# Optimization experiments

Measured on AMD Instinct MI355X. Metric: run time of the kernel, lower is better.

The kernel has to match this reference:

```python
import jax, jax.numpy as jnp
import numpy as np

B, S, D = 4, 1568, 1024
H = 16
HD = D // H  # 64


def setup_inputs() -> dict:
    key = jax.random.key(0)
    ks = jax.random.split(key, 9)
    scale = 0.02
    return {
        "hidden_states": jax.random.normal(ks[0], (B, S, D), dtype=jnp.float32),
        "Wq": jax.random.normal(ks[1], (D, D), dtype=jnp.float32) * scale,
        "bq": jnp.zeros((D,), dtype=jnp.float32),
        "Wk": jax.random.normal(ks[2], (D, D), dtype=jnp.float32) * scale,
        "bk": jnp.zeros((D,), dtype=jnp.float32),
        "Wv": jax.random.normal(ks[3], (D, D), dtype=jnp.float32) * scale,
        "bv": jnp.zeros((D,), dtype=jnp.float32),
        "Wp": jax.random.normal(ks[4], (D, D), dtype=jnp.float32) * scale,
        "bp": jnp.zeros((D,), dtype=jnp.float32),
    }


def reference(hidden_states, Wq, bq, Wk, bk, Wv, bv, Wp, bp):
    x = hidden_states  # [B, S, D]
    # Linear projections (torch Linear: x @ W.T + b)
    q = x @ Wq.T + bq
    k = x @ Wk.T + bk
    v = x @ Wv.T + bv
    # split heads: [B, H, S, HD]
    def heads(t):
        return t.reshape(B, S, H, HD).transpose(0, 2, 1, 3)
    q, k, v = heads(q), heads(k), heads(v)
    scale = 1.0 / jnp.sqrt(jnp.asarray(HD, dtype=q.dtype))
    scores = jnp.einsum('bhqd,bhkd->bhqk', q, k) * scale  # [B,H,S,S]
    probs = jax.nn.softmax(scores, axis=-1)
    ctx = jnp.einsum('bhqk,bhkd->bhqd', probs, v)  # [B,H,S,HD]
    ctx = ctx.transpose(0, 2, 1, 3).reshape(B, S, D)
    out = ctx @ Wp.T + bp
    return out
```

## Files before the change

### kernel.cpp

```cpp
#include <hip/hip_runtime.h>
#include <stdint.h>

#define SEQ 1568
#define SEQV 1600
#define DIM 1024
#define NB 4
#define NH 16
#define HD 64

typedef unsigned short u16;
typedef __bf16 bf16x8 __attribute__((ext_vector_type(8)));
typedef float f32x4 __attribute__((ext_vector_type(4)));

#define QSCALE 0.18033688011112042f

#define PSTR 72

__device__ __forceinline__ void load_lds16(const u16* g, u16* s) {
  __builtin_amdgcn_global_load_lds((__attribute__((address_space(1))) void*)g,
                                   (__attribute__((address_space(3))) void*)s,
                                   16, 0, 0);
}

__global__ __launch_bounds__(256) void cvt_all(
    const float* __restrict__ x,  const float* __restrict__ wq,
    const float* __restrict__ wk, const float* __restrict__ wv,
    const float* __restrict__ wp,
    u16* __restrict__ xb, u16* __restrict__ wqb, u16* __restrict__ wkb,
    u16* __restrict__ wvb, u16* __restrict__ wpb) {
  int i = blockIdx.x * 256 + threadIdx.x;
  const float* src; u16* dst; int off;
  if (i < 1605632)      { src = x;  dst = xb;  off = i; }
  else if (i < 1867776) { src = wq; dst = wqb; off = i - 1605632; }
  else if (i < 2129920) { src = wk; dst = wkb; off = i - 1867776; }
  else if (i < 2392064) { src = wv; dst = wvb; off = i - 2129920; }
  else                  { src = wp; dst = wpb; off = i - 2392064; }
  float4 v = ((const float4*)src)[off];
  union { unsigned long long u; __bf16 h[4]; } o;
  o.h[0] = (__bf16)v.x; o.h[1] = (__bf16)v.y;
  o.h[2] = (__bf16)v.z; o.h[3] = (__bf16)v.w;
  ((unsigned long long*)dst)[off] = o.u;
}

__global__ __launch_bounds__(256) void gemm_qkv(
    const u16* __restrict__ xb,
    const u16* __restrict__ wq, const u16* __restrict__ wk, const u16* __restrict__ wv,
    const float* __restrict__ bq, const float* __restrict__ bk, const float* __restrict__ bv,
    u16* __restrict__ qo, u16* __restrict__ ko, u16* __restrict__ vto) {
  const int z = blockIdx.z;
  const u16* W = (z == 0) ? wq : (z == 1) ? wk : wv;
  const float* bias = (z == 0) ? bq : (z == 1) ? bk : bv;

  __shared__ __align__(16) u16 sA[128 * 32];
  __shared__ __align__(16) u16 sB[128 * 32];

  const int tid = threadIdx.x;
  const int wave = tid >> 6;
  const int lane = tid & 63;
  const int l15 = lane & 15;
  const int quad = lane >> 4;
  const int bi = blockIdx.y / 13;
  const int st = blockIdx.y % 13;
  const int bn = blockIdx.x * 128;
  const int wm = (wave >> 1) * 64;
  const int wn = (wave & 1) * 64;

  const int sr = lane >> 2;
  const int sc = (lane & 3) * 8;
  const int r0 = wave * 32;

  f32x4 acc[4][4] = {};

  for (int k0 = 0; k0 < DIM; k0 += 32) {
    __syncthreads();
    {
      int sr1 = st * 128 + r0 + sr;       if (sr1 >= SEQ) sr1 = SEQ - 1;
      int sr2 = st * 128 + r0 + 16 + sr;  if (sr2 >= SEQ) sr2 = SEQ - 1;
      load_lds16(xb + (size_t)(bi * SEQ + sr1) * DIM + k0 + sc, &sA[r0 * 32]);
      load_lds16(xb + (size_t)(bi * SEQ + sr2) * DIM + k0 + sc, &sA[(r0 + 16) * 32]);
      const u16* gB = W + (size_t)(bn + r0 + sr) * DIM + k0 + sc;
      load_lds16(gB, &sB[r0 * 32]);
      load_lds16(gB + 16 * DIM, &sB[(r0 + 16) * 32]);
    }
    __syncthreads();

    bf16x8 a[4], b[4];
#pragma unroll
    for (int mt = 0; mt < 4; mt++)
      a[mt] = *(const bf16x8*)&sA[(wm + mt * 16 + l15) * 32 + quad * 8];
#pragma unroll
    for (int nt = 0; nt < 4; nt++)
      b[nt] = *(const bf16x8*)&sB[(wn + nt * 16 + l15) * 32 + quad * 8];
#pragma unroll
    for (int mt = 0; mt < 4; mt++)
#pragma unroll
      for (int nt = 0; nt < 4; nt++)
        acc[mt][nt] = __builtin_amdgcn_mfma_f32_16x16x32_bf16(a[mt], b[nt], acc[mt][nt], 0, 0, 0);
  }

#pragma unroll
  for (int nt = 0; nt < 4; nt++) {
    const int n = bn + wn + nt * 16 + l15;
    const float bia = bias[n];
    const int h = n >> 6, d = n & 63;
#pragma unroll
    for (int mt = 0; mt < 4; mt++) {
      const int sbase = st * 128 + wm + mt * 16 + quad * 4;
#pragma unroll
      for (int r = 0; r < 4; r++) {
        const int s = sbase + r;
        if (s < SEQ) {
          float val = acc[mt][nt][r] + bia;
          if (z == 0) val *= QSCALE;
          const __bf16 o = (__bf16)val;
          if (z == 0)
            *(__bf16*)&qo[(((size_t)(bi * NH + h)) * SEQ + s) * HD + d] = o;
          else if (z == 1)
            *(__bf16*)&ko[(((size_t)(bi * NH + h)) * SEQ + s) * HD + d] = o;
          else
            *(__bf16*)&vto[(((size_t)(bi * NH + h)) * HD + d) * SEQV + s] = o;
        }
      }
    }
  }
}

__global__ __launch_bounds__(256, 4) void attn(
    const u16* __restrict__ q, const u16* __restrict__ k,
    const u16* __restrict__ vt, u16* __restrict__ ctx) {
  const int bh = blockIdx.y;
  const int qt = blockIdx.x;
  const int tid = threadIdx.x;
  const int wave = tid >> 6, lane = tid & 63, l15 = lane & 15, quad = lane >> 4;

  __shared__ __align__(16) u16 sK[64 * 64];
  __shared__ __align__(16) u16 sV[64 * 64];
  __shared__ __align__(16) u16 sP[4][32 * PSTR];

  const u16* qh = q + (size_t)bh * (SEQ * HD);
  const u16* kh = k + (size_t)bh * (SEQ * HD);
  const u16* vh = vt + (size_t)bh * (HD * SEQV);

  bf16x8 aq[2][2];
#pragma unroll
  for (int mt = 0; mt < 2; mt++) {
    int qrow = qt * 128 + wave * 32 + mt * 16 + l15;
    int qr = qrow < SEQ ? qrow : SEQ - 1;
    aq[mt][0] = *(const bf16x8*)&qh[(size_t)qr * HD + quad * 8];
    aq[mt][1] = *(const bf16x8*)&qh[(size_t)qr * HD + 32 + quad * 8];
  }

  f32x4 o[2][4] = {};
  float lrow[2][4] = {};

  const int jrow = lane >> 3;
  const int cg = (lane & 7) ^ jrow;
  u16* sPw = sP[wave];
  const int j7 = l15 & 7;

  for (int j0 = 0; j0 < 1536; j0 += 64) {
    __syncthreads();
    load_lds16(&kh[(size_t)(j0 + wave * 16 + jrow) * HD + cg * 8], &sK[(wave * 16) * 64]);
    load_lds16(&kh[(size_t)(j0 + wave * 16 + 8 + jrow) * HD + cg * 8], &sK[(wave * 16 + 8) * 64]);
    load_lds16(&vh[(size_t)(wave * 16 + jrow) * SEQV + j0 + cg * 8], &sV[(wave * 16) * 64]);
    load_lds16(&vh[(size_t)(wave * 16 + 8 + jrow) * SEQV + j0 + cg * 8], &sV[(wave * 16 + 8) * 64]);
    __syncthreads();

#pragma unroll
    for (int mt = 0; mt < 2; mt++) {
      f32x4 s[4];
#pragma unroll
      for (int jt = 0; jt < 4; jt++) {
        const int j = jt * 16 + l15;
        bf16x8 b0 = *(const bf16x8*)&sK[j * 64 + ((quad ^ j7) * 8)];
        bf16x8 b1 = *(const bf16x8*)&sK[j * 64 + (((4 + quad) ^ j7) * 8)];
        f32x4 acc = {};
        acc = __builtin_amdgcn_mfma_f32_16x16x32_bf16(aq[mt][0], b0, acc, 0, 0, 0);
        acc = __builtin_amdgcn_mfma_f32_16x16x32_bf16(aq[mt][1], b1, acc, 0, 0, 0);
        s[jt] = acc;
      }
#pragma unroll
      for (int jt = 0; jt < 4; jt++)
#pragma unroll
        for (int r = 0; r < 4; r++) {
          float p = __builtin_exp2f(s[jt][r]);
          lrow[mt][r] += p;
          *(__bf16*)&sPw[(mt * 16 + quad * 4 + r) * PSTR + jt * 16 + l15] = (__bf16)p;
        }
    }

    asm volatile("s_waitcnt lgkmcnt(0)" ::: "memory");

#pragma unroll
    for (int kc = 0; kc < 2; kc++) {
      bf16x8 ap0 = *(const bf16x8*)&sPw[l15 * PSTR + kc * 32 + quad * 8];
      bf16x8 ap1 = *(const bf16x8*)&sPw[(16 + l15) * PSTR + kc * 32 + quad * 8];
#pragma unroll
      for (int dt = 0; dt < 4; dt++) {
        const int d7 = l15 & 7;
        bf16x8 bv = *(const bf16x8*)&sV[(dt * 16 + l15) * 64 + (((kc * 4 + quad) ^ d7) * 8)];
        o[0][dt] = __builtin_amdgcn_mfma_f32_16x16x32_bf16(ap0, bv, o[0][dt], 0, 0, 0);
        o[1][dt] = __builtin_amdgcn_mfma_f32_16x16x32_bf16(ap1, bv, o[1][dt], 0, 0, 0);
      }
    }
  }

  {
    const int j0 = 1536;
    __syncthreads();
    if (wave < 2) {
      load_lds16(&kh[(size_t)(j0 + wave * 16 + jrow) * HD + cg * 8], &sK[(wave * 16) * 64]);
      load_lds16(&kh[(size_t)(j0 + wave * 16 + 8 + jrow) * HD + cg * 8], &sK[(wave * 16 + 8) * 64]);
    }
    load_lds16(&vh[(size_t)(wave * 16 + jrow) * SEQV + j0 + cg * 8], &sV[(wave * 16) * 64]);
    load_lds16(&vh[(size_t)(wave * 16 + 8 + jrow) * SEQV + j0 + cg * 8], &sV[(wave * 16 + 8) * 64]);
    __syncthreads();

#pragma unroll
    for (int mt = 0; mt < 2; mt++) {
      f32x4 s[2];
#pragma unroll
      for (int jt = 0; jt < 2; jt++) {
        const int j = jt * 16 + l15;
        bf16x8 b0 = *(const bf16x8*)&sK[j * 64 + ((quad ^ j7) * 8)];
        bf16x8 b1 = *(const bf16x8*)&sK[j * 64 + (((4 + quad) ^ j7) * 8)];
        f32x4 acc = {};
        acc = __builtin_amdgcn_mfma_f32_16x16x32_bf16(aq[mt][0], b0, acc, 0, 0, 0);
        acc = __builtin_amdgcn_mfma_f32_16x16x32_bf16(aq[mt][1], b1, acc, 0, 0, 0);
        s[jt] = acc;
      }
#pragma unroll
      for (int jt = 0; jt < 2; jt++)
#pragma unroll
        for (int r = 0; r < 4; r++) {
          float p = __builtin_exp2f(s[jt][r]);
          lrow[mt][r] += p;
          *(__bf16*)&sPw[(mt * 16 + quad * 4 + r) * PSTR + jt * 16 + l15] = (__bf16)p;
        }
    }

    asm volatile("s_waitcnt lgkmcnt(0)" ::: "memory");

    {
      bf16x8 ap0 = *(const bf16x8*)&sPw[l15 * PSTR + quad * 8];
      bf16x8 ap1 = *(const bf16x8*)&sPw[(16 + l15) * PSTR + quad * 8];
#pragma unroll
      for (int dt = 0; dt < 4; dt++) {
        const int d7 = l15 & 7;
        bf16x8 bv = *(const bf16x8*)&sV[(dt * 16 + l15) * 64 + ((quad ^ d7) * 8)];
        o[0][dt] = __builtin_amdgcn_mfma_f32_16x16x32_bf16(ap0, bv, o[0][dt], 0, 0, 0);
        o[1][dt] = __builtin_amdgcn_mfma_f32_16x16x32_bf16(ap1, bv, o[1][dt], 0, 0, 0);
      }
    }
  }

  const int bi = bh >> 4, h = bh & 15;
#pragma unroll
  for (int mt = 0; mt < 2; mt++) {
#pragma unroll
    for (int r = 0; r < 4; r++) {
      float l = lrow[mt][r];
#pragma unroll
      for (int off = 8; off >= 1; off >>= 1) l += __shfl_xor(l, off, 16);
      const int srow = qt * 128 + wave * 32 + mt * 16 + quad * 4 + r;
      if (srow < SEQ) {
        const float inv = 1.0f / l;
#pragma unroll
        for (int dt = 0; dt < 4; dt++)
          *(__bf16*)&ctx[((size_t)(bi * SEQ + srow)) * DIM + h * HD + dt * 16 + l15] =
              (__bf16)(o[mt][dt][r] * inv);
      }
    }
  }
}

__global__ __launch_bounds__(256) void gemm_out(
    const u16* __restrict__ ctx, const u16* __restrict__ wp,
    const float* __restrict__ bp, float* __restrict__ out) {
  __shared__ __align__(16) u16 sA[128 * 32];
  __shared__ __align__(16) u16 sB[128 * 32];

  const int tid = threadIdx.x;
  const int wave = tid >> 6;
  const int lane = tid & 63;
  const int l15 = lane & 15;
  const int quad = lane >> 4;
  const int bm = blockIdx.y * 128;
  const int bn = blockIdx.x * 128;
  const int wm = (wave >> 1) * 64;
  const int wn = (wave & 1) * 64;
  const int sr = lane >> 2;
  const int sc = (lane & 3) * 8;
  const int r0 = wave * 32;

  f32x4 acc[4][4] = {};

  for (int k0 = 0; k0 < DIM; k0 += 32) {
    __syncthreads();
    {
      const u16* gA = ctx + (size_t)(bm + r0 + sr) * DIM + k0 + sc;
      load_lds16(gA, &sA[r0 * 32]);
      load_lds16(gA + 16 * DIM, &sA[(r0 + 16) * 32]);
      const u16* gB = wp + (size_t)(bn + r0 + sr) * DIM + k0 + sc;
      load_lds16(gB, &sB[r0 * 32]);
      load_lds16(gB + 16 * DIM, &sB[(r0 + 16) * 32]);
    }
    __syncthreads();

    bf16x8 a[4], b[4];
#pragma unroll
    for (int mt = 0; mt < 4; mt++)
      a[mt] = *(const bf16x8*)&sA[(wm + mt * 16 + l15) * 32 + quad * 8];
#pragma unroll
    for (int nt = 0; nt < 4; nt++)
      b[nt] = *(const bf16x8*)&sB[(wn + nt * 16 + l15) * 32 + quad * 8];
#pragma unroll
    for (int mt = 0; mt < 4; mt++)
#pragma unroll
      for (int nt = 0; nt < 4; nt++)
        acc[mt][nt] = __builtin_amdgcn_mfma_f32_16x16x32_bf16(a[mt], b[nt], acc[mt][nt], 0, 0, 0);
  }

#pragma unroll
  for (int nt = 0; nt < 4; nt++) {
    const int n = bn + wn + nt * 16 + l15;
    const float bia = bp[n];
#pragma unroll
    for (int mt = 0; mt < 4; mt++) {
      const int mbase = bm + wm + mt * 16 + quad * 4;
#pragma unroll
      for (int r = 0; r < 4; r++)
        out[(size_t)(mbase + r) * DIM + n] = acc[mt][nt][r] + bia;
    }
  }
}

extern "C" void kernel_launch(void* const* d_in, const int* in_sizes, int n_in,
                              void* d_out, int out_size, void* d_ws, size_t ws_size,
                              hipStream_t stream) {
  const float* x  = (const float*)d_in[0];
  const float* Wq = (const float*)d_in[1];
  const float* bq = (const float*)d_in[2];
  const float* Wk = (const float*)d_in[3];
  const float* bk = (const float*)d_in[4];
  const float* Wv = (const float*)d_in[5];
  const float* bv = (const float*)d_in[6];
  const float* Wp = (const float*)d_in[7];
  const float* bp = (const float*)d_in[8];
  float* out = (float*)d_out;

  char* ws = (char*)d_ws;
  u16* xb   = (u16*)(ws + 0);
  u16* wqb  = (u16*)(ws + 12845056);
  u16* wkb  = (u16*)(ws + 14942208);
  u16* wvb  = (u16*)(ws + 17039360);
  u16* wpb  = (u16*)(ws + 19136512);
  u16* qb   = (u16*)(ws + 21233664);
  u16* kb   = (u16*)(ws + 34078720);
  u16* vtb  = (u16*)(ws + 46923776);
  u16* ctxb = (u16*)(ws + 60030976);

  cvt_all<<<10368, 256, 0, stream>>>(x, Wq, Wk, Wv, Wp, xb, wqb, wkb, wvb, wpb);
  gemm_qkv<<<dim3(8, 52, 3), 256, 0, stream>>>(xb, wqb, wkb, wvb, bq, bk, bv, qb, kb, vtb);
  attn<<<dim3(13, 64), 256, 0, stream>>>(qb, kb, vtb, ctxb);
  gemm_out<<<dim3(8, 49), 256, 0, stream>>>(ctxb, wpb, bp, out);
}
```

Before: 297.7 us.

## Use BK=64 with XOR-swizzled LDS in projection GEMMs and halve out-GEMM M tile

Both the QKV and output projection GEMMs now stage a 64-wide K slice per iteration instead of 32. This halves the number of barrier pairs and loop iterations. Rows in LDS are laid out with an XOR swizzle on 16-byte column groups, which avoids bank conflicts when the MFMA fragments are read. The output GEMM tile shrinks from 128x128 to 64x128, doubling the grid to 784 blocks for better CU occupancy, at the cost of reloading the weight tile more often.

```diff
diff --git a/kernel.cpp b/kernel.cpp
--- a/kernel.cpp
+++ b/kernel.cpp
@@ -51,8 +51,8 @@
   const u16* W = (z == 0) ? wq : (z == 1) ? wk : wv;
   const float* bias = (z == 0) ? bq : (z == 1) ? bk : bv;
 
-  __shared__ __align__(16) u16 sA[128 * 32];
-  __shared__ __align__(16) u16 sB[128 * 32];
+  __shared__ __align__(16) u16 sA[128 * 64];
+  __shared__ __align__(16) u16 sB[128 * 64];
 
   const int tid = threadIdx.x;
   const int wave = tid >> 6;
@@ -65,37 +65,48 @@
   const int wm = (wave >> 1) * 64;
   const int wn = (wave & 1) * 64;
 
-  const int sr = lane >> 2;
-  const int sc = (lane & 3) * 8;
+  const int jrow = lane >> 3;
+  const int cg = (lane & 7) ^ jrow;
+  const int j7 = l15 & 7;
   const int r0 = wave * 32;
 
   f32x4 acc[4][4] = {};
 
-  for (int k0 = 0; k0 < DIM; k0 += 32) {
-    __syncthreads();
-    {
-      int sr1 = st * 128 + r0 + sr;       if (sr1 >= SEQ) sr1 = SEQ - 1;
-      int sr2 = st * 128 + r0 + 16 + sr;  if (sr2 >= SEQ) sr2 = SEQ - 1;
-      load_lds16(xb + (size_t)(bi * SEQ + sr1) * DIM + k0 + sc, &sA[r0 * 32]);
-      load_lds16(xb + (size_t)(bi * SEQ + sr2) * DIM + k0 + sc, &sA[(r0 + 16) * 32]);
-      const u16* gB = W + (size_t)(bn + r0 + sr) * DIM + k0 + sc;
-      load_lds16(gB, &sB[r0 * 32]);
-      load_lds16(gB + 16 * DIM, &sB[(r0 + 16) * 32]);
-    }
-    __syncthreads();
-
-    bf16x8 a[4], b[4];
-#pragma unroll
-    for (int mt = 0; mt < 4; mt++)
-      a[mt] = *(const bf16x8*)&sA[(wm + mt * 16 + l15) * 32 + quad * 8];
-#pragma unroll
-    for (int nt = 0; nt < 4; nt++)
-      b[nt] = *(const bf16x8*)&sB[(wn + nt * 16 + l15) * 32 + quad * 8];
-#pragma unroll
-    for (int mt = 0; mt < 4; mt++)
+  for (int k0 = 0; k0 < DIM; k0 += 64) {
+    __syncthreads();
+#pragma unroll
+    for (int i = 0; i < 4; i++) {
+      int srow = st * 128 + r0 + i * 8 + jrow;
+      if (srow >= SEQ) srow = SEQ - 1;
+      load_lds16(xb + (size_t)(bi * SEQ + srow) * DIM + k0 + cg * 8,
+                 &sA[(r0 + i * 8) * 64]);
+    }
+#pragma unroll
+    for (int i = 0; i < 4; i++)
+      load_lds16(W + (size_t)(bn + r0 + i * 8 + jrow) * DIM + k0 + cg * 8,
+                 &sB[(r0 + i * 8) * 64]);
+    __syncthreads();
+
+    bf16x8 a[2][4], b[2][4];
+#pragma unroll
+    for (int kk = 0; kk < 2; kk++) {
+#pragma unroll
+      for (int mt = 0; mt < 4; mt++)
+        a[kk][mt] = *(const bf16x8*)&sA[(wm + mt * 16 + l15) * 64 +
+                                        (((kk * 4 + quad) ^ j7) * 8)];
 #pragma unroll
       for (int nt = 0; nt < 4; nt++)
-        acc[mt][nt] = __builtin_amdgcn_mfma_f32_16x16x32_bf16(a[mt], b[nt], acc[mt][nt], 0, 0, 0);
+        b[kk][nt] = *(const bf16x8*)&sB[(wn + nt * 16 + l15) * 64 +
+                                        (((kk * 4 + quad) ^ j7) * 8)];
+    }
+#pragma unroll
+    for (int kk = 0; kk < 2; kk++)
+#pragma unroll
+      for (int mt = 0; mt < 4; mt++)
+#pragma unroll
+        for (int nt = 0; nt < 4; nt++)
+          acc[mt][nt] = __builtin_amdgcn_mfma_f32_16x16x32_bf16(
+              a[kk][mt], b[kk][nt], acc[mt][nt], 0, 0, 0);
   }
 
 #pragma unroll
@@ -277,48 +288,59 @@
 __global__ __launch_bounds__(256) void gemm_out(
     const u16* __restrict__ ctx, const u16* __restrict__ wp,
     const float* __restrict__ bp, float* __restrict__ out) {
-  __shared__ __align__(16) u16 sA[128 * 32];
-  __shared__ __align__(16) u16 sB[128 * 32];
+  __shared__ __align__(16) u16 sA[64 * 64];
+  __shared__ __align__(16) u16 sB[128 * 64];
 
   const int tid = threadIdx.x;
   const int wave = tid >> 6;
   const int lane = tid & 63;
   const int l15 = lane & 15;
   const int quad = lane >> 4;
-  const int bm = blockIdx.y * 128;
+  const int bm = blockIdx.y * 64;
   const int bn = blockIdx.x * 128;
-  const int wm = (wave >> 1) * 64;
+  const int wm = (wave >> 1) * 32;
   const int wn = (wave & 1) * 64;
-  const int sr = lane >> 2;
-  const int sc = (lane & 3) * 8;
-  const int r0 = wave * 32;
-
-  f32x4 acc[4][4] = {};
-
-  for (int k0 = 0; k0 < DIM; k0 += 32) {
-    __syncthreads();
-    {
-      const u16* gA = ctx + (size_t)(bm + r0 + sr) * DIM + k0 + sc;
-      load_lds16(gA, &sA[r0 * 32]);
-      load_lds16(gA + 16 * DIM, &sA[(r0 + 16) * 32]);
-      const u16* gB = wp + (size_t)(bn + r0 + sr) * DIM + k0 + sc;
-      load_lds16(gB, &sB[r0 * 32]);
-      load_lds16(gB + 16 * DIM, &sB[(r0 + 16) * 32]);
-    }
-    __syncthreads();
-
-    bf16x8 a[4], b[4];
-#pragma unroll
-    for (int mt = 0; mt < 4; mt++)
-      a[mt] = *(const bf16x8*)&sA[(wm + mt * 16 + l15) * 32 + quad * 8];
-#pragma unroll
-    for (int nt = 0; nt < 4; nt++)
-      b[nt] = *(const bf16x8*)&sB[(wn + nt * 16 + l15) * 32 + quad * 8];
-#pragma unroll
-    for (int mt = 0; mt < 4; mt++)
+
+  const int jrow = lane >> 3;
+  const int cg = (lane & 7) ^ jrow;
+  const int j7 = l15 & 7;
+  const int r0a = wave * 16;
+  const int r0b = wave * 32;
+
+  f32x4 acc[2][4] = {};
+
+  for (int k0 = 0; k0 < DIM; k0 += 64) {
+    __syncthreads();
+#pragma unroll
+    for (int i = 0; i < 2; i++)
+      load_lds16(ctx + (size_t)(bm + r0a + i * 8 + jrow) * DIM + k0 + cg * 8,
+                 &sA[(r0a + i * 8) * 64]);
+#pragma unroll
+    for (int i = 0; i < 4; i++)
+      load_lds16(wp + (size_t)(bn + r0b + i * 8 + jrow) * DIM + k0 + cg * 8,
+                 &sB[(r0b + i * 8) * 64]);
+    __syncthreads();
+
+    bf16x8 a[2][2], b[2][4];
+#pragma unroll
+    for (int kk = 0; kk < 2; kk++) {
+#pragma unroll
+      for (int mt = 0; mt < 2; mt++)
+        a[kk][mt] = *(const bf16x8*)&sA[(wm + mt * 16 + l15) * 64 +
+                                        (((kk * 4 + quad) ^ j7) * 8)];
 #pragma unroll
       for (int nt = 0; nt < 4; nt++)
-        acc[mt][nt] = __builtin_amdgcn_mfma_f32_16x16x32_bf16(a[mt], b[nt], acc[mt][nt], 0, 0, 0);
+        b[kk][nt] = *(const bf16x8*)&sB[(wn + nt * 16 + l15) * 64 +
+                                        (((kk * 4 + quad) ^ j7) * 8)];
+    }
+#pragma unroll
+    for (int kk = 0; kk < 2; kk++)
+#pragma unroll
+      for (int mt = 0; mt < 2; mt++)
+#pragma unroll
+        for (int nt = 0; nt < 4; nt++)
+          acc[mt][nt] = __builtin_amdgcn_mfma_f32_16x16x32_bf16(
+              a[kk][mt], b[kk][nt], acc[mt][nt], 0, 0, 0);
   }
 
 #pragma unroll
@@ -326,7 +348,7 @@
     const int n = bn + wn + nt * 16 + l15;
     const float bia = bp[n];
 #pragma unroll
-    for (int mt = 0; mt < 4; mt++) {
+    for (int mt = 0; mt < 2; mt++) {
       const int mbase = bm + wm + mt * 16 + quad * 4;
 #pragma unroll
       for (int r = 0; r < 4; r++)
@@ -363,5 +385,5 @@
   cvt_all<<<10368, 256, 0, stream>>>(x, Wq, Wk, Wv, Wp, xb, wqb, wkb, wvb, wpb);
   gemm_qkv<<<dim3(8, 52, 3), 256, 0, stream>>>(xb, wqb, wkb, wvb, bq, bk, bv, qb, kb, vtb);
   attn<<<dim3(13, 64), 256, 0, stream>>>(qb, kb, vtb, ctxb);
-  gemm_out<<<dim3(8, 49), 256, 0, stream>>>(ctxb, wpb, bp, out);
-}
+  gemm_out<<<dim3(8, 98), 256, 0, stream>>>(ctxb, wpb, bp, out);
+}
```

Result: slower. 315.3 us (+5.9%).

## Double-buffer QKV GEMM LDS tiles with BK=64 and XOR swizzle

Applied to the files above, without the earlier changes.

Rewrites the QKV projection GEMM main loop to use two LDS buffers, so the next K-tile's global->LDS loads are issued before computing on the current one, with one barrier per iteration instead of two. The K tile grows from 32 to 64, and an XOR column swizzle is applied to avoid LDS bank conflicts on fragment reads. It aims to hide global load latency and cut the number of synchronizations. The cost is four times the LDS (64KB), which may reduce occupancy.

```diff
diff --git a/kernel.cpp b/kernel.cpp
--- a/kernel.cpp
+++ b/kernel.cpp
@@ -51,8 +51,8 @@
   const u16* W = (z == 0) ? wq : (z == 1) ? wk : wv;
   const float* bias = (z == 0) ? bq : (z == 1) ? bk : bv;
 
-  __shared__ __align__(16) u16 sA[128 * 32];
-  __shared__ __align__(16) u16 sB[128 * 32];
+  __shared__ __align__(16) u16 sA[2][128 * 64];
+  __shared__ __align__(16) u16 sB[2][128 * 64];
 
   const int tid = threadIdx.x;
   const int wave = tid >> 6;
@@ -65,38 +65,57 @@
   const int wm = (wave >> 1) * 64;
   const int wn = (wave & 1) * 64;
 
-  const int sr = lane >> 2;
-  const int sc = (lane & 3) * 8;
+  const int jrow = lane >> 3;
+  const int cg = (lane & 7) ^ jrow;
+  const int j7 = l15 & 7;
   const int r0 = wave * 32;
 
+#define QKV_STAGE(cb, K0)                                                     \
+  do {                                                                        \
+    _Pragma("unroll") for (int i_ = 0; i_ < 4; i_++) {                        \
+      int srow_ = st * 128 + r0 + i_ * 8 + jrow;                              \
+      if (srow_ >= SEQ) srow_ = SEQ - 1;                                      \
+      load_lds16(xb + (size_t)(bi * SEQ + srow_) * DIM + (K0) + cg * 8,       \
+                 &sA[cb][(r0 + i_ * 8) * 64]);                                \
+    }                                                                         \
+    _Pragma("unroll") for (int i_ = 0; i_ < 4; i_++)                          \
+      load_lds16(W + (size_t)(bn + r0 + i_ * 8 + jrow) * DIM + (K0) + cg * 8, \
+                 &sB[cb][(r0 + i_ * 8) * 64]);                                \
+  } while (0)
+
   f32x4 acc[4][4] = {};
 
-  for (int k0 = 0; k0 < DIM; k0 += 32) {
-    __syncthreads();
-    {
-      int sr1 = st * 128 + r0 + sr;       if (sr1 >= SEQ) sr1 = SEQ - 1;
-      int sr2 = st * 128 + r0 + 16 + sr;  if (sr2 >= SEQ) sr2 = SEQ - 1;
-      load_lds16(xb + (size_t)(bi * SEQ + sr1) * DIM + k0 + sc, &sA[r0 * 32]);
-      load_lds16(xb + (size_t)(bi * SEQ + sr2) * DIM + k0 + sc, &sA[(r0 + 16) * 32]);
-      const u16* gB = W + (size_t)(bn + r0 + sr) * DIM + k0 + sc;
-      load_lds16(gB, &sB[r0 * 32]);
-      load_lds16(gB + 16 * DIM, &sB[(r0 + 16) * 32]);
-    }
-    __syncthreads();
-
-    bf16x8 a[4], b[4];
-#pragma unroll
-    for (int mt = 0; mt < 4; mt++)
-      a[mt] = *(const bf16x8*)&sA[(wm + mt * 16 + l15) * 32 + quad * 8];
-#pragma unroll
-    for (int nt = 0; nt < 4; nt++)
-      b[nt] = *(const bf16x8*)&sB[(wn + nt * 16 + l15) * 32 + quad * 8];
-#pragma unroll
-    for (int mt = 0; mt < 4; mt++)
+  QKV_STAGE(0, 0);
+  int cur = 0;
+  for (int it = 0; it < 16; it++) {
+    __syncthreads();
+    if (it < 15) QKV_STAGE(cur ^ 1, (it + 1) * 64);
+
+    const u16* A = &sA[cur][0];
+    const u16* Bt = &sB[cur][0];
+    bf16x8 a[2][4], b[2][4];
+#pragma unroll
+    for (int kk = 0; kk < 2; kk++) {
+#pragma unroll
+      for (int mt = 0; mt < 4; mt++)
+        a[kk][mt] = *(const bf16x8*)&A[(wm + mt * 16 + l15) * 64 +
+                                       (((kk * 4 + quad) ^ j7) * 8)];
 #pragma unroll
       for (int nt = 0; nt < 4; nt++)
-        acc[mt][nt] = __builtin_amdgcn_mfma_f32_16x16x32_bf16(a[mt], b[nt], acc[mt][nt], 0, 0, 0);
-  }
+        b[kk][nt] = *(const bf16x8*)&Bt[(wn + nt * 16 + l15) * 64 +
+                                        (((kk * 4 + quad) ^ j7) * 8)];
+    }
+#pragma unroll
+    for (int kk = 0; kk < 2; kk++)
+#pragma unroll
+      for (int mt = 0; mt < 4; mt++)
+#pragma unroll
+        for (int nt = 0; nt < 4; nt++)
+          acc[mt][nt] = __builtin_amdgcn_mfma_f32_16x16x32_bf16(
+              a[kk][mt], b[kk][nt], acc[mt][nt], 0, 0, 0);
+    cur ^= 1;
+  }
+#undef QKV_STAGE
 
 #pragma unroll
   for (int nt = 0; nt < 4; nt++) {
```

After: 314.8 us. +5.8%, slower.
